# Optimization experiments

Hardware: AMD Instinct MI355X
Metric: run time of the kernel (lower is better)

The kernel has to match this reference:

```python
import jax, jax.numpy as jnp
import numpy as np

# Static problem constants (must match setup_inputs)
NUM_GRAPHS = 64      # batch_size = int(batch[-1]) + 1
PTS_PER_GRAPH = 512
RATIO = 16           # centroids per graph
HEADS = 4
IN_CH = 64           # = out_channels per head (concat=False -> mean over heads)
NEG_SLOPE = 0.2


def setup_inputs() -> dict:
    key = jax.random.key(0)
    ks = jax.random.split(key, 8)
    N = NUM_GRAPHS * PTS_PER_GRAPH
    x = jax.random.normal(ks[0], (N, IN_CH), dtype=jnp.float32)
    edge_index = jnp.zeros((2, 2), dtype=jnp.int64)  # unused by forward
    batch = (jnp.arange(N) // PTS_PER_GRAPH).astype(jnp.int64)
    xcent_base = jax.random.normal(ks[1], (RATIO, IN_CH), dtype=jnp.float32)
    W_l = jax.random.normal(ks[2], (IN_CH, HEADS * IN_CH), dtype=jnp.float32) / np.sqrt(IN_CH)
    b_l = jax.random.normal(ks[3], (HEADS * IN_CH,), dtype=jnp.float32) * 0.01
    W_r = jax.random.normal(ks[4], (IN_CH, HEADS * IN_CH), dtype=jnp.float32) / np.sqrt(IN_CH)
    b_r = jax.random.normal(ks[5], (HEADS * IN_CH,), dtype=jnp.float32) * 0.01
    att = jax.random.normal(ks[6], (HEADS, IN_CH), dtype=jnp.float32) / np.sqrt(IN_CH)
    bias = jax.random.normal(ks[7], (IN_CH,), dtype=jnp.float32) * 0.01
    return {"x": x, "edge_index": edge_index, "batch": batch,
            "xcent_base": xcent_base, "W_l": W_l, "b_l": b_l,
            "W_r": W_r, "b_r": b_r, "att": att, "bias": bias}


def _bipart_pool(x, batch, xcent_base, W_l, b_l, W_r, b_r, att, bias):
    N = x.shape[0]
    B = NUM_GRAPHS
    Nc = B * RATIO  # number of centroid (target) nodes

    # Dense bipartite edges: each source node -> all RATIO centroids of its graph.
    src = jnp.repeat(jnp.arange(N, dtype=jnp.int32), RATIO)                     # [E]
    dst = jnp.tile(jnp.arange(RATIO, dtype=jnp.int32), N) \
        + jnp.repeat(batch.astype(jnp.int32), RATIO) * RATIO                    # [E]

    # PyG GATv2Conv(add_self_loops=True): remove src==dst edges, then add
    # self loops (i,i) for i < min(N_src, N_dst) = Nc. Keep static shapes by
    # masking the removed edges instead of deleting them.
    self_idx = jnp.arange(Nc, dtype=jnp.int32)
    src_f = jnp.concatenate([src, self_idx])
    dst_f = jnp.concatenate([dst, self_idx])
    drop = jnp.concatenate([src == dst, jnp.zeros((Nc,), dtype=bool)])          # [E+Nc]

    # Linear projections (source and target sides)
    x_l = (x @ W_l + b_l).reshape(N, HEADS, IN_CH)                              # [N,H,C]
    xcent = jnp.tile(xcent_base, (B, 1))                                        # [Nc,IN]
    x_r = (xcent @ W_r + b_r).reshape(Nc, HEADS, IN_CH)                         # [Nc,H,C]

    # GATv2 attention: leaky_relu(x_i + x_j) . att, softmax per target node
    xj = x_l[src_f]                                                             # [E',H,C]
    g = jax.nn.leaky_relu(xj + x_r[dst_f], NEG_SLOPE)
    alpha = jnp.einsum('ehc,hc->eh', g, att)                                    # [E',H]
    alpha = jnp.where(drop[:, None], jnp.float32(-1e30), alpha)
    amax = jax.ops.segment_max(alpha, dst_f, num_segments=Nc)                   # [Nc,H]
    e = jnp.exp(alpha - amax[dst_f])
    den = jax.ops.segment_sum(e, dst_f, num_segments=Nc)                        # [Nc,H]
    w = e / den[dst_f]                                                          # [E',H]

    out = jax.ops.segment_sum(w[..., None] * xj, dst_f, num_segments=Nc)        # [Nc,H,C]
    out = out.mean(axis=1) + bias                                               # concat=False -> mean heads
    return out.reshape(B, RATIO, IN_CH)


def reference(x, edge_index, batch, xcent_base, W_l, b_l, W_r, b_r, att, bias):
    xcent = _bipart_pool(x, batch, xcent_base, W_l, b_l, W_r, b_r, att, bias)
    batchcent = jnp.repeat(jnp.arange(NUM_GRAPHS, dtype=jnp.int64), RATIO)
    return xcent, batchcent
```

## Files before the change

kernel.cpp:

```cpp
#include <hip/hip_runtime.h>

#define PTS 512
#define CH  64
#define NC  1024

using s8v = __attribute__((ext_vector_type(8))) short;
using f4v = __attribute__((ext_vector_type(4))) float;

static __device__ __forceinline__ unsigned short f2b(float f) {
    unsigned u = __float_as_uint(f);
    return (unsigned short)((u + 0x7FFFu + ((u >> 16) & 1u)) >> 16);
}
static __device__ __forceinline__ float b2f(unsigned short s) {
    return __uint_as_float((unsigned)s << 16);
}

__global__ __launch_bounds__(256) void k0(
    const float* __restrict__ xcb, const float* __restrict__ W_r,
    const float* __restrict__ b_r, const float* __restrict__ att,
    const float* __restrict__ W_l,
    float* __restrict__ xr_ws, float* __restrict__ sxr_ws,
    unsigned short* __restrict__ Wt)
{
    __shared__ float s_row[256];
    const int blk = blockIdx.x, tid = threadIdx.x;
    if (blk < 16) {
        const int h = blk >> 2, rq = blk & 3;
        const int rl = tid >> 6, c = tid & 63;
        const int r = rq * 4 + rl;
        float acc = b_r[h * 64 + c];
        for (int k = 0; k < 64; ++k)
            acc = fmaf(xcb[r * 64 + k], W_r[k * 256 + h * 64 + c], acc);
        xr_ws[(h * 16 + r) * 64 + c] = acc;
        s_row[rl * 64 + c] = acc;
        __syncthreads();
        if (tid < 4) {
            float s = 0.f;
            for (int cc = 0; cc < 64; ++cc)
                s = fmaf(s_row[tid * 64 + cc], att[h * 64 + cc], s);
            sxr_ws[h * 16 + rq * 4 + tid] = s;
        }
    } else {
        int base = (blk - 16) * 2048;
        for (int t = tid; t < 2048; t += 256) {
            int idx = base + t;
            int h = idx >> 12, ch = (idx >> 6) & 63, k = idx & 63;
            Wt[idx] = f2b(W_l[k * 256 + h * 64 + ch]);
        }
    }
}

__global__ __launch_bounds__(256, 2) void k1(
    const float* __restrict__ x, const unsigned short* __restrict__ Wt,
    const float* __restrict__ b_l, const float* __restrict__ att,
    const float* __restrict__ xr_ws, const float* __restrict__ sxr_ws,
    const float* __restrict__ bias,
    float* __restrict__ aws, unsigned short* __restrict__ xlself,
    float* __restrict__ out)
{
    __shared__ unsigned short s_xl[64 * 264];

    const int tid = threadIdx.x;
    const int lane = tid & 63;
    const int w = __builtin_amdgcn_readfirstlane(tid >> 6);
    const int blk = blockIdx.x;
    const int row0 = blk * 64;
    const int l15 = lane & 15, quad = lane >> 4;

    f4v acc[4][4];
    const f4v zf = {0.f, 0.f, 0.f, 0.f};
#pragma unroll
    for (int m = 0; m < 4; ++m)
#pragma unroll
        for (int n = 0; n < 4; ++n) acc[m][n] = zf;

#pragma unroll
    for (int ks = 0; ks < 2; ++ks) {
        s8v Af[4], Bf[4];
#pragma unroll
        for (int m = 0; m < 4; ++m) {
            const float* xp = x + (size_t)(row0 + m * 16 + l15) * 64 + ks * 32 + quad * 8;
            float4 u0 = *(const float4*)xp;
            float4 u1 = *(const float4*)(xp + 4);
            s8v a;
            a[0] = (short)f2b(u0.x); a[1] = (short)f2b(u0.y);
            a[2] = (short)f2b(u0.z); a[3] = (short)f2b(u0.w);
            a[4] = (short)f2b(u1.x); a[5] = (short)f2b(u1.y);
            a[6] = (short)f2b(u1.z); a[7] = (short)f2b(u1.w);
            Af[m] = a;
        }
#pragma unroll
        for (int n = 0; n < 4; ++n)
            Bf[n] = *(const s8v*)(Wt + (size_t)(w * 64 + n * 16 + l15) * 64
                                  + ks * 32 + quad * 8);
#pragma unroll
        for (int m = 0; m < 4; ++m)
#pragma unroll
            for (int n = 0; n < 4; ++n)
                acc[m][n] = __builtin_amdgcn_mfma_f32_16x16x32_bf16(
                    Af[m], Bf[n], acc[m][n], 0, 0, 0);
    }

    float blv[4];
#pragma unroll
    for (int n = 0; n < 4; ++n) blv[n] = b_l[w * 64 + n * 16 + l15];
#pragma unroll
    for (int m = 0; m < 4; ++m)
#pragma unroll
        for (int n = 0; n < 4; ++n) {
            int ch = w * 64 + n * 16 + l15;
#pragma unroll
            for (int qq = 0; qq < 4; ++qq) {
                int row = m * 16 + quad * 4 + qq;
                s_xl[row * 264 + ch] = f2b(acc[m][n][qq] + blv[n]);
            }
        }

    if (blk >= 16 && blk < 20) {
        int base = (blk - 16) * 16384;
        float bv = bias[tid & 63];
#pragma unroll
        for (int j = 0; j < 64; ++j) out[base + j * 256 + tid] = bv;
    }
    if (blk == 20) {
#pragma unroll
        for (int j = 0; j < 4; ++j) {
            int c = j * 256 + tid;
            out[65536 + c] = (float)(c >> 4);
        }
    }

    __syncthreads();

    if (blk < 16) {
#pragma unroll
        for (int t = 0; t < 8; ++t) {
            int idx = tid + t * 256;
            int row = idx >> 5, co = (idx & 31) * 8;
            uint4 v = *(const uint4*)&s_xl[row * 264 + co];
            *(uint4*)&xlself[(size_t)(row0 + row) * 256 + co] = v;
        }
    }

    const float* attw = att + w * 64;
    const float* xrw  = xr_ws + w * 1024;
    float ac[16];
#pragma unroll
    for (int r = 0; r < 16; ++r) ac[r] = 0.f;
    float sxl = 0.f;

#pragma unroll
    for (int half = 0; half < 2; ++half) {
        const int cb = half * 32;
        float xlv[32], atv[32];
#pragma unroll
        for (int c8 = 0; c8 < 4; ++c8) {
            uint4 raw = *(const uint4*)&s_xl[lane * 264 + w * 64 + cb + c8 * 8];
            unsigned uu[4] = {raw.x, raw.y, raw.z, raw.w};
#pragma unroll
            for (int p = 0; p < 4; ++p) {
                xlv[c8 * 8 + 2 * p]     = __uint_as_float(uu[p] << 16);
                xlv[c8 * 8 + 2 * p + 1] = __uint_as_float(uu[p] & 0xffff0000u);
            }
        }
#pragma unroll
        for (int cq = 0; cq < 8; ++cq) {
            float4 a4 = *(const float4*)(attw + cb + cq * 4);
            atv[cq * 4 + 0] = a4.x; atv[cq * 4 + 1] = a4.y;
            atv[cq * 4 + 2] = a4.z; atv[cq * 4 + 3] = a4.w;
        }
#pragma unroll
        for (int t = 0; t < 32; ++t) sxl = fmaf(atv[t], xlv[t], sxl);

#pragma unroll 2
        for (int r = 0; r < 16; ++r) {
            const float4* xrp = (const float4*)(xrw + r * 64 + cb);
            float a = 0.f;
#pragma unroll
            for (int cq = 0; cq < 8; ++cq) {
                float4 x4 = xrp[cq];
                a = fmaf(atv[cq * 4 + 0], fabsf(xlv[cq * 4 + 0] + x4.x), a);
                a = fmaf(atv[cq * 4 + 1], fabsf(xlv[cq * 4 + 1] + x4.y), a);
                a = fmaf(atv[cq * 4 + 2], fabsf(xlv[cq * 4 + 2] + x4.z), a);
                a = fmaf(atv[cq * 4 + 3], fabsf(xlv[cq * 4 + 3] + x4.w), a);
            }
            ac[r] += a;
        }
    }

    float* ap = aws + ((size_t)(blk >> 3) * 4 + w) * 8192 + (blk & 7) * 64 + lane;
#pragma unroll
    for (int r = 0; r < 16; ++r)
        ap[r * 512] = 0.6f * (sxl + sxr_ws[w * 16 + r]) + 0.4f * ac[r];
}

__global__ __launch_bounds__(512, 1) void k2(
    const float* __restrict__ x, const float* __restrict__ W_l,
    const float* __restrict__ b_l, const float* __restrict__ aws,
    const unsigned short* __restrict__ xlself, float* __restrict__ out)
{
    __shared__ float s_et[8192];
    __shared__ float sW[4096];
    __shared__ float s_y[1024];
    __shared__ float s_m[16], s_inv[16], s_f[16];

    const int bh = blockIdx.x, b = bh >> 2, h = bh & 3;
    const int tid = threadIdx.x;
    const float* abh = aws + (size_t)bh * 8192;

    for (int idx = tid; idx < 4096; idx += 512)
        sW[idx] = W_l[(idx >> 6) * 256 + h * 64 + (idx & 63)];
    for (int idx = tid; idx < 8192; idx += 512) {
        int r = idx >> 9, i = idx & 511;
        s_et[i * 16 + r] = abh[idx];
    }

    {
        const int r = tid >> 5, lg = tid & 31;
        const int snode = b * 16 + r;
        const float a_self = aws[(size_t)((snode >> 9) * 4 + h) * 8192
                                 + r * 512 + (snode & 511)];
        float m = a_self;
        for (int j = 0; j < 16; ++j) {
            int i = lg + j * 32;
            float a = abh[r * 512 + i];
            if (b == 0 && i == r) a = -1e30f;
            m = fmaxf(m, a);
        }
#pragma unroll
        for (int off = 16; off >= 1; off >>= 1) m = fmaxf(m, __shfl_xor(m, off));
        float d = 0.f;
        for (int j = 0; j < 16; ++j) {
            int i = lg + j * 32;
            float a = abh[r * 512 + i];
            d += (b == 0 && i == r) ? 0.f : __expf(a - m);
        }
#pragma unroll
        for (int off = 16; off >= 1; off >>= 1) d += __shfl_xor(d, off);
        if (lg == 0) {
            float es = __expf(a_self - m);
            float inv = 1.f / (d + es);
            s_m[r] = m; s_inv[r] = inv; s_f[r] = es * inv;
        }
    }
    __syncthreads();

    for (int idx = tid; idx < 8192; idx += 512) {
        int i = idx >> 4, r = idx & 15;
        float a = s_et[idx];
        float e = (b == 0 && i == r) ? 0.f : __expf(a - s_m[r]) * s_inv[r];
        s_et[idx] = e;
    }
    __syncthreads();

    const int kt = tid & 15, rt = (tid >> 4) & 3, is = tid >> 6;
    float y4[4][4];
#pragma unroll
    for (int i = 0; i < 4; ++i)
#pragma unroll
        for (int j = 0; j < 4; ++j) y4[i][j] = 0.f;

    const float* xb = x + ((size_t)b * PTS + is * 64) * 64;
#pragma unroll 4
    for (int ii = 0; ii < 64; ++ii) {
        float4 xv = *(const float4*)(xb + ii * 64 + kt * 4);
        float4 ev = *(const float4*)&s_et[(is * 64 + ii) * 16 + rt * 4];
        y4[0][0] = fmaf(ev.x, xv.x, y4[0][0]); y4[0][1] = fmaf(ev.x, xv.y, y4[0][1]);
        y4[0][2] = fmaf(ev.x, xv.z, y4[0][2]); y4[0][3] = fmaf(ev.x, xv.w, y4[0][3]);
        y4[1][0] = fmaf(ev.y, xv.x, y4[1][0]); y4[1][1] = fmaf(ev.y, xv.y, y4[1][1]);
        y4[1][2] = fmaf(ev.y, xv.z, y4[1][2]); y4[1][3] = fmaf(ev.y, xv.w, y4[1][3]);
        y4[2][0] = fmaf(ev.z, xv.x, y4[2][0]); y4[2][1] = fmaf(ev.z, xv.y, y4[2][1]);
        y4[2][2] = fmaf(ev.z, xv.z, y4[2][2]); y4[2][3] = fmaf(ev.z, xv.w, y4[2][3]);
        y4[3][0] = fmaf(ev.w, xv.x, y4[3][0]); y4[3][1] = fmaf(ev.w, xv.y, y4[3][1]);
        y4[3][2] = fmaf(ev.w, xv.z, y4[3][2]); y4[3][3] = fmaf(ev.w, xv.w, y4[3][3]);
    }
    __syncthreads();

#pragma unroll
    for (int rr = 0; rr < 4; ++rr)
        *(float4*)&s_et[is * 1024 + (rt * 4 + rr) * 64 + kt * 4] =
            make_float4(y4[rr][0], y4[rr][1], y4[rr][2], y4[rr][3]);
    __syncthreads();

    for (int o = tid; o < 1024; o += 512) {
        float s = 0.f;
#pragma unroll
        for (int sl = 0; sl < 8; ++sl) s += s_et[sl * 1024 + o];
        s_y[o] = s;
    }
    __syncthreads();

    for (int o = tid; o < 1024; o += 512) {
        int r = o >> 6, ch = o & 63;
        float a = 0.f;
#pragma unroll
        for (int k = 0; k < 64; ++k)
            a = fmaf(s_y[r * 64 + k], sW[k * 64 + ch], a);
        float f = s_f[r];
        float val = a + (1.f - f) * b_l[h * 64 + ch]
                  + f * b2f(xlself[(size_t)(b * 16 + r) * 256 + h * 64 + ch]);
        atomicAdd(&out[(b * 16 + r) * 64 + ch], 0.25f * val);
    }
}

extern "C" void kernel_launch(void* const* d_in, const int* in_sizes, int n_in,
                              void* d_out, int out_size, void* d_ws, size_t ws_size,
                              hipStream_t stream) {
    (void)in_sizes; (void)n_in; (void)out_size; (void)ws_size;
    const float* x    = (const float*)d_in[0];
    const float* xcb  = (const float*)d_in[3];
    const float* W_l  = (const float*)d_in[4];
    const float* b_l  = (const float*)d_in[5];
    const float* W_r  = (const float*)d_in[6];
    const float* b_r  = (const float*)d_in[7];
    const float* att  = (const float*)d_in[8];
    const float* bias = (const float*)d_in[9];
    float* out = (float*)d_out;

    float* wsf = (float*)d_ws;
    float*          aws    = wsf;
    float*          xr_ws  = wsf + 2097152;
    float*          sxr_ws = wsf + 2101248;
    unsigned short* Wt     = (unsigned short*)(wsf + 2101376);
    unsigned short* xlself = (unsigned short*)(wsf + 2109568);

    hipLaunchKernelGGL(k0, dim3(24), dim3(256), 0, stream,
                       xcb, W_r, b_r, att, W_l, xr_ws, sxr_ws, Wt);
    hipLaunchKernelGGL(k1, dim3(512), dim3(256), 0, stream,
                       x, Wt, b_l, att, xr_ws, sxr_ws, bias, aws, xlself, out);
    hipLaunchKernelGGL(k2, dim3(256), dim3(512), 0, stream,
                       x, W_l, b_l, aws, xlself, out);
}
```

Baseline: 119.3 us.

## Split k2 over four point-quarters per graph-head, reducing partials with atomics

k2 now launches 1024 blocks of 256 threads instead of 256 blocks of 512. Each block handles one quarter of the 512 source points for a (graph, head) pair, so more CUs are occupied and LDS use per block is smaller. Softmax statistics are computed redundantly in every quarter block, and the exponentials are written straight into LDS only for that quarter. The partial products are projected through W_l separately and combined via atomicAdd into the output, which adds 4x projection work and 4x atomics. The bias and self-loop terms are added only by quarter 0.

After: 133.8 us. +12.2%, slower.

```diff
diff --git a/kernel.cpp b/kernel.cpp
--- a/kernel.cpp
+++ b/kernel.cpp
@@ -194,62 +194,56 @@
         ap[r * 512] = 0.6f * (sxl + sxr_ws[w * 16 + r]) + 0.4f * ac[r];
 }
 
-__global__ __launch_bounds__(512, 1) void k2(
+__global__ __launch_bounds__(256, 4) void k2(
     const float* __restrict__ x, const float* __restrict__ W_l,
     const float* __restrict__ b_l, const float* __restrict__ aws,
     const unsigned short* __restrict__ xlself, float* __restrict__ out)
 {
-    __shared__ float s_et[8192];
+    __shared__ float s_et[2048];
+    __shared__ float s_p[3072];
     __shared__ float sW[4096];
-    __shared__ float s_y[1024];
-    __shared__ float s_m[16], s_inv[16], s_f[16];
-
-    const int bh = blockIdx.x, b = bh >> 2, h = bh & 3;
+    __shared__ float s_f[16];
+
+    const int q = blockIdx.x & 3, h = (blockIdx.x >> 2) & 3, b = blockIdx.x >> 4;
     const int tid = threadIdx.x;
-    const float* abh = aws + (size_t)bh * 8192;
-
-    for (int idx = tid; idx < 4096; idx += 512)
+    const float* abh = aws + (size_t)(b * 4 + h) * 8192;
+
+    for (int idx = tid; idx < 4096; idx += 256)
         sW[idx] = W_l[(idx >> 6) * 256 + h * 64 + (idx & 63)];
-    for (int idx = tid; idx < 8192; idx += 512) {
-        int r = idx >> 9, i = idx & 511;
-        s_et[i * 16 + r] = abh[idx];
-    }
 
     {
-        const int r = tid >> 5, lg = tid & 31;
+        const int r = tid >> 4, lg = tid & 15;
         const int snode = b * 16 + r;
         const float a_self = aws[(size_t)((snode >> 9) * 4 + h) * 8192
                                  + r * 512 + (snode & 511)];
         float m = a_self;
-        for (int j = 0; j < 16; ++j) {
-            int i = lg + j * 32;
+        for (int j = 0; j < 32; ++j) {
+            int i = lg + j * 16;
             float a = abh[r * 512 + i];
             if (b == 0 && i == r) a = -1e30f;
             m = fmaxf(m, a);
         }
 #pragma unroll
-        for (int off = 16; off >= 1; off >>= 1) m = fmaxf(m, __shfl_xor(m, off));
+        for (int off = 8; off >= 1; off >>= 1) m = fmaxf(m, __shfl_xor(m, off));
         float d = 0.f;
-        for (int j = 0; j < 16; ++j) {
-            int i = lg + j * 32;
+        for (int j = 0; j < 32; ++j) {
+            int i = lg + j * 16;
             float a = abh[r * 512 + i];
             d += (b == 0 && i == r) ? 0.f : __expf(a - m);
         }
 #pragma unroll
-        for (int off = 16; off >= 1; off >>= 1) d += __shfl_xor(d, off);
-        if (lg == 0) {
-            float es = __expf(a_self - m);
-            float inv = 1.f / (d + es);
-            s_m[r] = m; s_inv[r] = inv; s_f[r] = es * inv;
-        }
-    }
-    __syncthreads();
-
-    for (int idx = tid; idx < 8192; idx += 512) {
-        int i = idx >> 4, r = idx & 15;
-        float a = s_et[idx];
-        float e = (b == 0 && i == r) ? 0.f : __expf(a - s_m[r]) * s_inv[r];
-        s_et[idx] = e;
+        for (int off = 8; off >= 1; off >>= 1) d += __shfl_xor(d, off);
+        const float es = __expf(a_self - m);
+        const float inv = 1.f / (d + es);
+        if (lg == 0) s_f[r] = es * inv;
+
+        for (int j = 0; j < 8; ++j) {
+            int iloc = lg + j * 16;
+            int i = q * 128 + iloc;
+            float a = abh[r * 512 + i];
+            bool drop = (b == 0) && (i == r);
+            s_et[iloc * 16 + r] = drop ? 0.f : __expf(a - m) * inv;
+        }
     }
     __syncthreads();
 
@@ -260,11 +254,11 @@
 #pragma unroll
         for (int j = 0; j < 4; ++j) y4[i][j] = 0.f;
 
-    const float* xb = x + ((size_t)b * PTS + is * 64) * 64;
+    const float* xbq = x + ((size_t)b * PTS + q * 128 + is * 32) * 64;
 #pragma unroll 4
-    for (int ii = 0; ii < 64; ++ii) {
-        float4 xv = *(const float4*)(xb + ii * 64 + kt * 4);
-        float4 ev = *(const float4*)&s_et[(is * 64 + ii) * 16 + rt * 4];
+    for (int i = 0; i < 32; ++i) {
+        float4 xv = *(const float4*)(xbq + i * 64 + kt * 4);
+        float4 ev = *(const float4*)&s_et[(is * 32 + i) * 16 + rt * 4];
         y4[0][0] = fmaf(ev.x, xv.x, y4[0][0]); y4[0][1] = fmaf(ev.x, xv.y, y4[0][1]);
         y4[0][2] = fmaf(ev.x, xv.z, y4[0][2]); y4[0][3] = fmaf(ev.x, xv.w, y4[0][3]);
         y4[1][0] = fmaf(ev.y, xv.x, y4[1][0]); y4[1][1] = fmaf(ev.y, xv.y, y4[1][1]);
@@ -274,32 +268,53 @@
         y4[3][0] = fmaf(ev.w, xv.x, y4[3][0]); y4[3][1] = fmaf(ev.w, xv.y, y4[3][1]);
         y4[3][2] = fmaf(ev.w, xv.z, y4[3][2]); y4[3][3] = fmaf(ev.w, xv.w, y4[3][3]);
     }
+
+    if (is > 0) {
+#pragma unroll
+        for (int rr = 0; rr < 4; ++rr)
+            *(float4*)&s_p[((is - 1) * 64 + rt * 16 + kt) * 16 + rr * 4] =
+                make_float4(y4[rr][0], y4[rr][1], y4[rr][2], y4[rr][3]);
+    }
     __syncthreads();
-
-#pragma unroll
-    for (int rr = 0; rr < 4; ++rr)
-        *(float4*)&s_et[is * 1024 + (rt * 4 + rr) * 64 + kt * 4] =
-            make_float4(y4[rr][0], y4[rr][1], y4[rr][2], y4[rr][3]);
+    float* s_yq = s_et;
+    if (is == 0) {
+#pragma unroll
+        for (int j = 0; j < 3; ++j)
+#pragma unroll
+            for (int rr = 0; rr < 4; ++rr) {
+                float4 v = *(const float4*)&s_p[(j * 64 + rt * 16 + kt) * 16 + rr * 4];
+                y4[rr][0] += v.x; y4[rr][1] += v.y; y4[rr][2] += v.z; y4[rr][3] += v.w;
+            }
+#pragma unroll
+        for (int rr = 0; rr < 4; ++rr)
+            *(float4*)&s_yq[(rt * 4 + rr) * 64 + kt * 4] =
+                make_float4(y4[rr][0], y4[rr][1], y4[rr][2], y4[rr][3]);
+    }
     __syncthreads();
 
-    for (int o = tid; o < 1024; o += 512) {
-        float s = 0.f;
-#pragma unroll
-        for (int sl = 0; sl < 8; ++sl) s += s_et[sl * 1024 + o];
-        s_y[o] = s;
-    }
-    __syncthreads();
-
-    for (int o = tid; o < 1024; o += 512) {
-        int r = o >> 6, ch = o & 63;
-        float a = 0.f;
-#pragma unroll
-        for (int k = 0; k < 64; ++k)
-            a = fmaf(s_y[r * 64 + k], sW[k * 64 + ch], a);
-        float f = s_f[r];
-        float val = a + (1.f - f) * b_l[h * 64 + ch]
-                  + f * b2f(xlself[(size_t)(b * 16 + r) * 256 + h * 64 + ch]);
-        atomicAdd(&out[(b * 16 + r) * 64 + ch], 0.25f * val);
+    {
+        const int r2 = tid >> 4, ch = (tid & 15) * 4;
+        float o0 = 0.f, o1 = 0.f, o2 = 0.f, o3 = 0.f;
+#pragma unroll
+        for (int k = 0; k < 64; ++k) {
+            float yv = s_yq[r2 * 64 + k];
+            float4 wv = *(const float4*)&sW[k * 64 + ch];
+            o0 = fmaf(yv, wv.x, o0); o1 = fmaf(yv, wv.y, o1);
+            o2 = fmaf(yv, wv.z, o2); o3 = fmaf(yv, wv.w, o3);
+        }
+        if (q == 0) {
+            const float f = s_f[r2];
+            const float* blp = b_l + h * 64 + ch;
+            const unsigned short* xsp =
+                xlself + (size_t)(b * 16 + r2) * 256 + h * 64 + ch;
+            o0 += (1.f - f) * blp[0] + f * b2f(xsp[0]);
+            o1 += (1.f - f) * blp[1] + f * b2f(xsp[1]);
+            o2 += (1.f - f) * blp[2] + f * b2f(xsp[2]);
+            o3 += (1.f - f) * blp[3] + f * b2f(xsp[3]);
+        }
+        float* op = out + (b * 16 + r2) * 64 + ch;
+        atomicAdd(op + 0, 0.25f * o0); atomicAdd(op + 1, 0.25f * o1);
+        atomicAdd(op + 2, 0.25f * o2); atomicAdd(op + 3, 0.25f * o3);
     }
 }
 
@@ -328,6 +343,6 @@
                        xcb, W_r, b_r, att, W_l, xr_ws, sxr_ws, Wt);
     hipLaunchKernelGGL(k1, dim3(512), dim3(256), 0, stream,
                        x, Wt, b_l, att, xr_ws, sxr_ws, bias, aws, xlself, out);
-    hipLaunchKernelGGL(k2, dim3(256), dim3(512), 0, stream,
+    hipLaunchKernelGGL(k2, dim3(1024), dim3(256), 0, stream,
                        x, W_l, b_l, aws, xlself, out);
 }
```

## Fuse x_l projection and attention scoring into the per-(graph,head) softmax kernel

Applied to the files above, without the earlier changes.

Merges k1 and k2 into a single kernel launched per (graph, head). Each block recomputes its own x_l tile with MFMA and computes the attention logits locally. The self-loop x_l rows are computed in-block, so the xlself workspace round trip goes away, and the output bias initialisation moves into k0. This removes one launch and the cross-kernel dependency. In exchange, logits still pass through global memory within the block, the per-block work is serialised over two halves, and parallelism per block drops.

Measured after the change: 140.7 us. 1.18x slower.

```diff
diff --git a/kernel.cpp b/kernel.cpp
--- a/kernel.cpp
+++ b/kernel.cpp
@@ -11,16 +11,15 @@
     unsigned u = __float_as_uint(f);
     return (unsigned short)((u + 0x7FFFu + ((u >> 16) & 1u)) >> 16);
 }
-static __device__ __forceinline__ float b2f(unsigned short s) {
-    return __uint_as_float((unsigned)s << 16);
-}
+static __device__ __forceinline__ float blo(unsigned u) { return __uint_as_float(u << 16); }
+static __device__ __forceinline__ float bhi(unsigned u) { return __uint_as_float(u & 0xffff0000u); }
 
 __global__ __launch_bounds__(256) void k0(
     const float* __restrict__ xcb, const float* __restrict__ W_r,
     const float* __restrict__ b_r, const float* __restrict__ att,
-    const float* __restrict__ W_l,
+    const float* __restrict__ W_l, const float* __restrict__ bias,
     float* __restrict__ xr_ws, float* __restrict__ sxr_ws,
-    unsigned short* __restrict__ Wt)
+    unsigned short* __restrict__ Wt, float* __restrict__ out)
 {
     __shared__ float s_row[256];
     const int blk = blockIdx.x, tid = threadIdx.x;
@@ -40,46 +39,65 @@
                 s = fmaf(s_row[tid * 64 + cc], att[h * 64 + cc], s);
             sxr_ws[h * 16 + rq * 4 + tid] = s;
         }
-    } else {
+    } else if (blk < 24) {
         int base = (blk - 16) * 2048;
         for (int t = tid; t < 2048; t += 256) {
             int idx = base + t;
             int h = idx >> 12, ch = (idx >> 6) & 63, k = idx & 63;
             Wt[idx] = f2b(W_l[k * 256 + h * 64 + ch]);
         }
+    } else {
+        int base = (blk - 24) * 16384;
+        float bv = bias[tid & 63];
+#pragma unroll
+        for (int j = 0; j < 64; ++j) out[base + j * 256 + tid] = bv;
+        if (blk == 27) {
+#pragma unroll
+            for (int j = 0; j < 4; ++j) {
+                int c = j * 256 + tid;
+                out[65536 + c] = (float)(c >> 4);
+            }
+        }
     }
 }
 
-__global__ __launch_bounds__(256, 2) void k1(
+__global__ __launch_bounds__(512, 2) void kmain(
     const float* __restrict__ x, const unsigned short* __restrict__ Wt,
-    const float* __restrict__ b_l, const float* __restrict__ att,
+    const float* __restrict__ W_l, const float* __restrict__ b_l,
+    const float* __restrict__ att,
     const float* __restrict__ xr_ws, const float* __restrict__ sxr_ws,
-    const float* __restrict__ bias,
-    float* __restrict__ aws, unsigned short* __restrict__ xlself,
-    float* __restrict__ out)
+    float* __restrict__ aws, float* __restrict__ out)
 {
-    __shared__ unsigned short s_xl[64 * 264];
-
+    __shared__ float s_region[10240];
+    __shared__ float sW[4096];
+    __shared__ float s_xls[1024];
+    __shared__ float s_as[16], s_m[16], s_inv[16], s_f[16];
+
+    unsigned short* s_xl = (unsigned short*)s_region;
+    float* s_et = s_region;
+
+    const int bh = blockIdx.x, b = bh >> 2, h = bh & 3;
     const int tid = threadIdx.x;
     const int lane = tid & 63;
-    const int w = __builtin_amdgcn_readfirstlane(tid >> 6);
-    const int blk = blockIdx.x;
-    const int row0 = blk * 64;
+    const int w = tid >> 6;
     const int l15 = lane & 15, quad = lane >> 4;
-
-    f4v acc[4][4];
-    const f4v zf = {0.f, 0.f, 0.f, 0.f};
-#pragma unroll
-    for (int m = 0; m < 4; ++m)
-#pragma unroll
-        for (int n = 0; n < 4; ++n) acc[m][n] = zf;
-
-#pragma unroll
-    for (int ks = 0; ks < 2; ++ks) {
-        s8v Af[4], Bf[4];
-#pragma unroll
-        for (int m = 0; m < 4; ++m) {
-            const float* xp = x + (size_t)(row0 + m * 16 + l15) * 64 + ks * 32 + quad * 8;
+    float* awsb = aws + (size_t)bh * 8192;
+
+    for (int idx = tid; idx < 4096; idx += 512)
+        sW[idx] = W_l[(idx >> 6) * 256 + h * 64 + (idx & 63)];
+
+    float blv[4];
+#pragma unroll
+    for (int n = 0; n < 4; ++n) blv[n] = b_l[h * 64 + n * 16 + l15];
+
+    if (w == 0) {
+        f4v accs[4];
+        const f4v zf = {0.f, 0.f, 0.f, 0.f};
+#pragma unroll
+        for (int n = 0; n < 4; ++n) accs[n] = zf;
+#pragma unroll
+        for (int ks = 0; ks < 2; ++ks) {
+            const float* xp = x + (size_t)(b * 16 + l15) * 64 + ks * 32 + quad * 8;
             float4 u0 = *(const float4*)xp;
             float4 u1 = *(const float4*)(xp + 4);
             s8v a;
@@ -87,143 +105,154 @@
             a[2] = (short)f2b(u0.z); a[3] = (short)f2b(u0.w);
             a[4] = (short)f2b(u1.x); a[5] = (short)f2b(u1.y);
             a[6] = (short)f2b(u1.z); a[7] = (short)f2b(u1.w);
-            Af[m] = a;
+#pragma unroll
+            for (int n = 0; n < 4; ++n) {
+                s8v bv = *(const s8v*)(Wt + (size_t)(h * 64 + n * 16 + l15) * 64
+                                       + ks * 32 + quad * 8);
+                accs[n] = __builtin_amdgcn_mfma_f32_16x16x32_bf16(a, bv, accs[n], 0, 0, 0);
+            }
         }
 #pragma unroll
         for (int n = 0; n < 4; ++n)
-            Bf[n] = *(const s8v*)(Wt + (size_t)(w * 64 + n * 16 + l15) * 64
-                                  + ks * 32 + quad * 8);
-#pragma unroll
-        for (int m = 0; m < 4; ++m)
-#pragma unroll
-            for (int n = 0; n < 4; ++n)
-                acc[m][n] = __builtin_amdgcn_mfma_f32_16x16x32_bf16(
-                    Af[m], Bf[n], acc[m][n], 0, 0, 0);
-    }
-
-    float blv[4];
-#pragma unroll
-    for (int n = 0; n < 4; ++n) blv[n] = b_l[w * 64 + n * 16 + l15];
-#pragma unroll
-    for (int m = 0; m < 4; ++m)
-#pragma unroll
-        for (int n = 0; n < 4; ++n) {
-            int ch = w * 64 + n * 16 + l15;
-#pragma unroll
-            for (int qq = 0; qq < 4; ++qq) {
-                int row = m * 16 + quad * 4 + qq;
-                s_xl[row * 264 + ch] = f2b(acc[m][n][qq] + blv[n]);
-            }
-        }
-
-    if (blk >= 16 && blk < 20) {
-        int base = (blk - 16) * 16384;
-        float bv = bias[tid & 63];
-#pragma unroll
-        for (int j = 0; j < 64; ++j) out[base + j * 256 + tid] = bv;
-    }
-    if (blk == 20) {
-#pragma unroll
-        for (int j = 0; j < 4; ++j) {
-            int c = j * 256 + tid;
-            out[65536 + c] = (float)(c >> 4);
-        }
-    }
-
-    __syncthreads();
-
-    if (blk < 16) {
-#pragma unroll
-        for (int t = 0; t < 8; ++t) {
-            int idx = tid + t * 256;
-            int row = idx >> 5, co = (idx & 31) * 8;
-            uint4 v = *(const uint4*)&s_xl[row * 264 + co];
-            *(uint4*)&xlself[(size_t)(row0 + row) * 256 + co] = v;
-        }
-    }
-
-    const float* attw = att + w * 64;
-    const float* xrw  = xr_ws + w * 1024;
-    float ac[16];
-#pragma unroll
-    for (int r = 0; r < 16; ++r) ac[r] = 0.f;
-    float sxl = 0.f;
-
-#pragma unroll
-    for (int half = 0; half < 2; ++half) {
-        const int cb = half * 32;
-        float xlv[32], atv[32];
-#pragma unroll
-        for (int c8 = 0; c8 < 4; ++c8) {
-            uint4 raw = *(const uint4*)&s_xl[lane * 264 + w * 64 + cb + c8 * 8];
-            unsigned uu[4] = {raw.x, raw.y, raw.z, raw.w};
-#pragma unroll
-            for (int p = 0; p < 4; ++p) {
-                xlv[c8 * 8 + 2 * p]     = __uint_as_float(uu[p] << 16);
-                xlv[c8 * 8 + 2 * p + 1] = __uint_as_float(uu[p] & 0xffff0000u);
-            }
-        }
-#pragma unroll
-        for (int cq = 0; cq < 8; ++cq) {
-            float4 a4 = *(const float4*)(attw + cb + cq * 4);
-            atv[cq * 4 + 0] = a4.x; atv[cq * 4 + 1] = a4.y;
-            atv[cq * 4 + 2] = a4.z; atv[cq * 4 + 3] = a4.w;
-        }
-#pragma unroll
-        for (int t = 0; t < 32; ++t) sxl = fmaf(atv[t], xlv[t], sxl);
-
+#pragma unroll
+            for (int qq = 0; qq < 4; ++qq)
+                s_xls[(quad * 4 + qq) * 64 + n * 16 + l15] = accs[n][qq] + blv[n];
+    }
+
+    const float* attw = att + h * 64;
+    const float* xrw  = xr_ws + h * 1024;
+
+#pragma unroll 1
+    for (int hg = 0; hg < 2; ++hg) {
+        {
+            f4v acc[2][4];
+            const f4v zf = {0.f, 0.f, 0.f, 0.f};
+#pragma unroll
+            for (int m = 0; m < 2; ++m)
+#pragma unroll
+                for (int n = 0; n < 4; ++n) acc[m][n] = zf;
+#pragma unroll
+            for (int ks = 0; ks < 2; ++ks) {
+                s8v Af[2], Bf[4];
+#pragma unroll
+                for (int m = 0; m < 2; ++m) {
+                    const float* xp = x + (size_t)(b * 512 + hg * 256 + w * 32
+                                     + m * 16 + l15) * 64 + ks * 32 + quad * 8;
+                    float4 u0 = *(const float4*)xp;
+                    float4 u1 = *(const float4*)(xp + 4);
+                    s8v a;
+                    a[0] = (short)f2b(u0.x); a[1] = (short)f2b(u0.y);
+                    a[2] = (short)f2b(u0.z); a[3] = (short)f2b(u0.w);
+                    a[4] = (short)f2b(u1.x); a[5] = (short)f2b(u1.y);
+                    a[6] = (short)f2b(u1.z); a[7] = (short)f2b(u1.w);
+                    Af[m] = a;
+                }
+#pragma unroll
+                for (int n = 0; n < 4; ++n)
+                    Bf[n] = *(const s8v*)(Wt + (size_t)(h * 64 + n * 16 + l15) * 64
+                                          + ks * 32 + quad * 8);
+#pragma unroll
+                for (int m = 0; m < 2; ++m)
+#pragma unroll
+                    for (int n = 0; n < 4; ++n)
+                        acc[m][n] = __builtin_amdgcn_mfma_f32_16x16x32_bf16(
+                            Af[m], Bf[n], acc[m][n], 0, 0, 0);
+            }
+#pragma unroll
+            for (int m = 0; m < 2; ++m)
+#pragma unroll
+                for (int n = 0; n < 4; ++n) {
+                    int ch = n * 16 + l15;
+#pragma unroll
+                    for (int qq = 0; qq < 4; ++qq) {
+                        int row = w * 32 + m * 16 + quad * 4 + qq;
+                        s_xl[row * 72 + ch] = f2b(acc[m][n][qq] + blv[n]);
+                    }
+                }
+        }
+        __syncthreads();
+
+        {
+            const int i_loc = tid >> 1, halfc = tid & 1, cb = halfc * 32;
+            float xlv[32], atv[32];
+#pragma unroll
+            for (int c8 = 0; c8 < 4; ++c8) {
+                uint4 raw = *(const uint4*)&s_xl[i_loc * 72 + cb + c8 * 8];
+                unsigned uu[4] = {raw.x, raw.y, raw.z, raw.w};
+#pragma unroll
+                for (int p = 0; p < 4; ++p) {
+                    xlv[c8 * 8 + 2 * p]     = blo(uu[p]);
+                    xlv[c8 * 8 + 2 * p + 1] = bhi(uu[p]);
+                }
+            }
+#pragma unroll
+            for (int cq = 0; cq < 8; ++cq) {
+                float4 a4 = *(const float4*)(attw + cb + cq * 4);
+                atv[cq * 4 + 0] = a4.x; atv[cq * 4 + 1] = a4.y;
+                atv[cq * 4 + 2] = a4.z; atv[cq * 4 + 3] = a4.w;
+            }
+            float sxl = 0.f;
+#pragma unroll
+            for (int t = 0; t < 32; ++t) sxl = fmaf(atv[t], xlv[t], sxl);
+
+            float ac[16];
+#pragma unroll
+            for (int r = 0; r < 16; ++r) ac[r] = 0.f;
 #pragma unroll 2
-        for (int r = 0; r < 16; ++r) {
-            const float4* xrp = (const float4*)(xrw + r * 64 + cb);
-            float a = 0.f;
-#pragma unroll
-            for (int cq = 0; cq < 8; ++cq) {
-                float4 x4 = xrp[cq];
-                a = fmaf(atv[cq * 4 + 0], fabsf(xlv[cq * 4 + 0] + x4.x), a);
-                a = fmaf(atv[cq * 4 + 1], fabsf(xlv[cq * 4 + 1] + x4.y), a);
-                a = fmaf(atv[cq * 4 + 2], fabsf(xlv[cq * 4 + 2] + x4.z), a);
-                a = fmaf(atv[cq * 4 + 3], fabsf(xlv[cq * 4 + 3] + x4.w), a);
-            }
-            ac[r] += a;
-        }
-    }
-
-    float* ap = aws + ((size_t)(blk >> 3) * 4 + w) * 8192 + (blk & 7) * 64 + lane;
-#pragma unroll
-    for (int r = 0; r < 16; ++r)
-        ap[r * 512] = 0.6f * (sxl + sxr_ws[w * 16 + r]) + 0.4f * ac[r];
-}
-
-__global__ __launch_bounds__(512, 1) void k2(
-    const float* __restrict__ x, const float* __restrict__ W_l,
-    const float* __restrict__ b_l, const float* __restrict__ aws,
-    const unsigned short* __restrict__ xlself, float* __restrict__ out)
-{
-    __shared__ float s_et[8192];
-    __shared__ float sW[4096];
-    __shared__ float s_y[1024];
-    __shared__ float s_m[16], s_inv[16], s_f[16];
-
-    const int bh = blockIdx.x, b = bh >> 2, h = bh & 3;
-    const int tid = threadIdx.x;
-    const float* abh = aws + (size_t)bh * 8192;
-
-    for (int idx = tid; idx < 4096; idx += 512)
-        sW[idx] = W_l[(idx >> 6) * 256 + h * 64 + (idx & 63)];
-    for (int idx = tid; idx < 8192; idx += 512) {
-        int r = idx >> 9, i = idx & 511;
-        s_et[i * 16 + r] = abh[idx];
-    }
+            for (int r = 0; r < 16; ++r) {
+                const float4* xrp = (const float4*)(xrw + r * 64 + cb);
+                float a = 0.f;
+#pragma unroll
+                for (int cq = 0; cq < 8; ++cq) {
+                    float4 x4 = xrp[cq];
+                    a = fmaf(atv[cq * 4 + 0], fabsf(xlv[cq * 4 + 0] + x4.x), a);
+                    a = fmaf(atv[cq * 4 + 1], fabsf(xlv[cq * 4 + 1] + x4.y), a);
+                    a = fmaf(atv[cq * 4 + 2], fabsf(xlv[cq * 4 + 2] + x4.z), a);
+                    a = fmaf(atv[cq * 4 + 3], fabsf(xlv[cq * 4 + 3] + x4.w), a);
+                }
+                ac[r] = a;
+            }
+            sxl += __shfl_xor(sxl, 1);
+#pragma unroll
+            for (int r = 0; r < 16; ++r) ac[r] += __shfl_xor(ac[r], 1);
+
+            const int i = hg * 256 + i_loc;
+            float* ap = awsb + (halfc * 8) * 512 + i;
+#pragma unroll
+            for (int r8 = 0; r8 < 8; ++r8) {
+                int r = halfc * 8 + r8;
+                ap[r8 * 512] = 0.6f * (sxl + sxr_ws[h * 16 + r]) + 0.4f * ac[r];
+            }
+        }
+        __syncthreads();
+    }
+
+    if (tid < 16) {
+        int r = tid;
+        float sxl_s = 0.f, acs = 0.f;
+#pragma unroll
+        for (int cq = 0; cq < 16; ++cq) {
+            float4 v4 = *(const float4*)&s_xls[r * 64 + cq * 4];
+            float4 a4 = *(const float4*)(attw + cq * 4);
+            float4 x4 = *(const float4*)(xrw + r * 64 + cq * 4);
+            sxl_s = fmaf(a4.x, v4.x, sxl_s); sxl_s = fmaf(a4.y, v4.y, sxl_s);
+            sxl_s = fmaf(a4.z, v4.z, sxl_s); sxl_s = fmaf(a4.w, v4.w, sxl_s);
+            acs = fmaf(a4.x, fabsf(v4.x + x4.x), acs);
+            acs = fmaf(a4.y, fabsf(v4.y + x4.y), acs);
+            acs = fmaf(a4.z, fabsf(v4.z + x4.z), acs);
+            acs = fmaf(a4.w, fabsf(v4.w + x4.w), acs);
+        }
+        s_as[r] = 0.6f * (sxl_s + sxr_ws[h * 16 + r]) + 0.4f * acs;
+    }
+    __syncthreads();
 
     {
         const int r = tid >> 5, lg = tid & 31;
-        const int snode = b * 16 + r;
-        const float a_self = aws[(size_t)((snode >> 9) * 4 + h) * 8192
-                                 + r * 512 + (snode & 511)];
+        const float a_self = s_as[r];
         float m = a_self;
         for (int j = 0; j < 16; ++j) {
             int i = lg + j * 32;
-            float a = abh[r * 512 + i];
+            float a = awsb[r * 512 + i];
             if (b == 0 && i == r) a = -1e30f;
             m = fmaxf(m, a);
         }
@@ -232,7 +261,7 @@
         float d = 0.f;
         for (int j = 0; j < 16; ++j) {
             int i = lg + j * 32;
-            float a = abh[r * 512 + i];
+            float a = awsb[r * 512 + i];
             d += (b == 0 && i == r) ? 0.f : __expf(a - m);
         }
 #pragma unroll
@@ -243,13 +272,20 @@
             s_m[r] = m; s_inv[r] = inv; s_f[r] = es * inv;
         }
     }
+    {
+        const int r = tid & 15, i0 = tid >> 4;
+        for (int k = 0; k < 16; ++k) {
+            int i = i0 + k * 32;
+            s_et[i * 20 + r] = awsb[r * 512 + i];
+        }
+    }
     __syncthreads();
 
     for (int idx = tid; idx < 8192; idx += 512) {
         int i = idx >> 4, r = idx & 15;
-        float a = s_et[idx];
+        float a = s_et[i * 20 + r];
         float e = (b == 0 && i == r) ? 0.f : __expf(a - s_m[r]) * s_inv[r];
-        s_et[idx] = e;
+        s_et[i * 20 + r] = e;
     }
     __syncthreads();
 
@@ -264,7 +300,7 @@
 #pragma unroll 4
     for (int ii = 0; ii < 64; ++ii) {
         float4 xv = *(const float4*)(xb + ii * 64 + kt * 4);
-        float4 ev = *(const float4*)&s_et[(is * 64 + ii) * 16 + rt * 4];
+        float4 ev = *(const float4*)&s_et[(is * 64 + ii) * 20 + rt * 4];
         y4[0][0] = fmaf(ev.x, xv.x, y4[0][0]); y4[0][1] = fmaf(ev.x, xv.y, y4[0][1]);
         y4[0][2] = fmaf(ev.x, xv.z, y4[0][2]); y4[0][3] = fmaf(ev.x, xv.w, y4[0][3]);
         y4[1][0] = fmaf(ev.y, xv.x, y4[1][0]); y4[1][1] = fmaf(ev.y, xv.y, y4[1][1]);
@@ -278,15 +314,15 @@
 
 #pragma unroll
     for (int rr = 0; rr < 4; ++rr)
-        *(float4*)&s_et[is * 1024 + (rt * 4 + rr) * 64 + kt * 4] =
+        *(float4*)&s_region[is * 1024 + (rt * 4 + rr) * 64 + kt * 4] =
             make_float4(y4[rr][0], y4[rr][1], y4[rr][2], y4[rr][3]);
     __syncthreads();
 
     for (int o = tid; o < 1024; o += 512) {
         float s = 0.f;
 #pragma unroll
-        for (int sl = 0; sl < 8; ++sl) s += s_et[sl * 1024 + o];
-        s_y[o] = s;
+        for (int sl = 0; sl < 8; ++sl) s += s_region[sl * 1024 + o];
+        s_region[8192 + o] = s;
     }
     __syncthreads();
 
@@ -295,10 +331,9 @@
         float a = 0.f;
 #pragma unroll
         for (int k = 0; k < 64; ++k)
-            a = fmaf(s_y[r * 64 + k], sW[k * 64 + ch], a);
+            a = fmaf(s_region[8192 + r * 64 + k], sW[k * 64 + ch], a);
         float f = s_f[r];
-        float val = a + (1.f - f) * b_l[h * 64 + ch]
-                  + f * b2f(xlself[(size_t)(b * 16 + r) * 256 + h * 64 + ch]);
+        float val = a + (1.f - f) * b_l[h * 64 + ch] + f * s_xls[r * 64 + ch];
         atomicAdd(&out[(b * 16 + r) * 64 + ch], 0.25f * val);
     }
 }
@@ -322,12 +357,9 @@
     float*          xr_ws  = wsf + 2097152;
     float*          sxr_ws = wsf + 2101248;
     unsigned short* Wt     = (unsigned short*)(wsf + 2101376);
-    unsigned short* xlself = (unsigned short*)(wsf + 2109568);
-
-    hipLaunchKernelGGL(k0, dim3(24), dim3(256), 0, stream,
-                       xcb, W_r, b_r, att, W_l, xr_ws, sxr_ws, Wt);
-    hipLaunchKernelGGL(k1, dim3(512), dim3(256), 0, stream,
-                       x, Wt, b_l, att, xr_ws, sxr_ws, bias, aws, xlself, out);
-    hipLaunchKernelGGL(k2, dim3(256), dim3(512), 0, stream,
-                       x, W_l, b_l, aws, xlself, out);
+
+    hipLaunchKernelGGL(k0, dim3(28), dim3(256), 0, stream,
+                       xcb, W_r, b_r, att, W_l, bias, xr_ws, sxr_ws, Wt, out);
+    hipLaunchKernelGGL(kmain, dim3(256), dim3(512), 0, stream,
+                       x, Wt, W_l, b_l, att, xr_ws, sxr_ws, aws, out);
 }
```

## Compute partial softmax max/sum in k1 and merge online in k2

Applied to the files above, without the earlier changes.

k1 now computes per-chunk max and exp-sum for each target row with wavefront reductions and writes them to new workspace buffers. k2 merges these partials with an online-softmax combine instead of reading the attention logits twice to find the max and denominator. The transpose into shared memory now uses a padded stride of 20 to cut LDS bank conflicts. In exchange k1 does extra shuffles and exps in its epilogue, and k2 uses more shared memory.

New measurement: 125.8 us. 1.06x slower.

```diff
diff --git a/kernel.cpp b/kernel.cpp
--- a/kernel.cpp
+++ b/kernel.cpp
@@ -56,7 +56,8 @@
     const float* __restrict__ xr_ws, const float* __restrict__ sxr_ws,
     const float* __restrict__ bias,
     float* __restrict__ aws, unsigned short* __restrict__ xlself,
-    float* __restrict__ out)
+    float* __restrict__ out,
+    float* __restrict__ sm_ws, float* __restrict__ ss_ws)
 {
     __shared__ unsigned short s_xl[64 * 264];
 
@@ -188,18 +189,40 @@
         }
     }
 
-    float* ap = aws + ((size_t)(blk >> 3) * 4 + w) * 8192 + (blk & 7) * 64 + lane;
-#pragma unroll
-    for (int r = 0; r < 16; ++r)
-        ap[r * 512] = 0.6f * (sxl + sxr_ws[w * 16 + r]) + 0.4f * ac[r];
+    float av[16];
+    const int bh = (blk >> 3) * 4 + w, chunk = blk & 7;
+    float* ap = aws + (size_t)bh * 8192 + chunk * 64 + lane;
+#pragma unroll
+    for (int r = 0; r < 16; ++r) {
+        av[r] = 0.6f * (sxl + sxr_ws[w * 16 + r]) + 0.4f * ac[r];
+        ap[r * 512] = av[r];
+    }
+
+    const bool maskblk = (row0 == 0);
+#pragma unroll 2
+    for (int r = 0; r < 16; ++r) {
+        float v = (maskblk && lane == r) ? -1e30f : av[r];
+        float m = v;
+#pragma unroll
+        for (int off = 32; off >= 1; off >>= 1) m = fmaxf(m, __shfl_xor(m, off));
+        float e = __expf(v - m);
+        float s = e;
+#pragma unroll
+        for (int off = 32; off >= 1; off >>= 1) s += __shfl_xor(s, off);
+        if (lane == r) {
+            sm_ws[((size_t)bh * 16 + r) * 8 + chunk] = m;
+            ss_ws[((size_t)bh * 16 + r) * 8 + chunk] = s;
+        }
+    }
 }
 
 __global__ __launch_bounds__(512, 1) void k2(
     const float* __restrict__ x, const float* __restrict__ W_l,
     const float* __restrict__ b_l, const float* __restrict__ aws,
+    const float* __restrict__ sm_ws, const float* __restrict__ ss_ws,
     const unsigned short* __restrict__ xlself, float* __restrict__ out)
 {
-    __shared__ float s_et[8192];
+    __shared__ float s_et[10240];
     __shared__ float sW[4096];
     __shared__ float s_y[1024];
     __shared__ float s_m[16], s_inv[16], s_f[16];
@@ -208,48 +231,39 @@
     const int tid = threadIdx.x;
     const float* abh = aws + (size_t)bh * 8192;
 
+    if (tid < 128) {
+        const int r = tid >> 3, c = tid & 7;
+        float m = sm_ws[((size_t)bh * 16 + r) * 8 + c];
+        float s = ss_ws[((size_t)bh * 16 + r) * 8 + c];
+#pragma unroll
+        for (int off = 1; off < 8; off <<= 1) {
+            float m2 = __shfl_xor(m, off);
+            float s2 = __shfl_xor(s, off);
+            float mm = fmaxf(m, m2);
+            s = s * __expf(m - mm) + s2 * __expf(m2 - mm);
+            m = mm;
+        }
+        if (c == 0) {
+            const int snode = b * 16 + r;
+            const float a_self = aws[(size_t)((snode >> 9) * 4 + h) * 8192
+                                     + r * 512 + (snode & 511)];
+            float mm = fmaxf(m, a_self);
+            float es = __expf(a_self - mm);
+            float den = s * __expf(m - mm) + es;
+            float inv = 1.f / den;
+            s_m[r] = mm; s_inv[r] = inv; s_f[r] = es * inv;
+        }
+    }
     for (int idx = tid; idx < 4096; idx += 512)
         sW[idx] = W_l[(idx >> 6) * 256 + h * 64 + (idx & 63)];
-    for (int idx = tid; idx < 8192; idx += 512) {
-        int r = idx >> 9, i = idx & 511;
-        s_et[i * 16 + r] = abh[idx];
-    }
-
-    {
-        const int r = tid >> 5, lg = tid & 31;
-        const int snode = b * 16 + r;
-        const float a_self = aws[(size_t)((snode >> 9) * 4 + h) * 8192
-                                 + r * 512 + (snode & 511)];
-        float m = a_self;
-        for (int j = 0; j < 16; ++j) {
-            int i = lg + j * 32;
-            float a = abh[r * 512 + i];
-            if (b == 0 && i == r) a = -1e30f;
-            m = fmaxf(m, a);
-        }
-#pragma unroll
-        for (int off = 16; off >= 1; off >>= 1) m = fmaxf(m, __shfl_xor(m, off));
-        float d = 0.f;
-        for (int j = 0; j < 16; ++j) {
-            int i = lg + j * 32;
-            float a = abh[r * 512 + i];
-            d += (b == 0 && i == r) ? 0.f : __expf(a - m);
-        }
-#pragma unroll
-        for (int off = 16; off >= 1; off >>= 1) d += __shfl_xor(d, off);
-        if (lg == 0) {
-            float es = __expf(a_self - m);
-            float inv = 1.f / (d + es);
-            s_m[r] = m; s_inv[r] = inv; s_f[r] = es * inv;
-        }
-    }
-    __syncthreads();
-
-    for (int idx = tid; idx < 8192; idx += 512) {
-        int i = idx >> 4, r = idx & 15;
-        float a = s_et[idx];
+    __syncthreads();
+
+    for (int k = 0; k < 16; ++k) {
+        int idx = k * 512 + tid;
+        int r = k, i = tid;
+        float a = abh[idx];
         float e = (b == 0 && i == r) ? 0.f : __expf(a - s_m[r]) * s_inv[r];
-        s_et[idx] = e;
+        s_et[i * 20 + r] = e;
     }
     __syncthreads();
 
@@ -264,7 +278,7 @@
 #pragma unroll 4
     for (int ii = 0; ii < 64; ++ii) {
         float4 xv = *(const float4*)(xb + ii * 64 + kt * 4);
-        float4 ev = *(const float4*)&s_et[(is * 64 + ii) * 16 + rt * 4];
+        float4 ev = *(const float4*)&s_et[(is * 64 + ii) * 20 + rt * 4];
         y4[0][0] = fmaf(ev.x, xv.x, y4[0][0]); y4[0][1] = fmaf(ev.x, xv.y, y4[0][1]);
         y4[0][2] = fmaf(ev.x, xv.z, y4[0][2]); y4[0][3] = fmaf(ev.x, xv.w, y4[0][3]);
         y4[1][0] = fmaf(ev.y, xv.x, y4[1][0]); y4[1][1] = fmaf(ev.y, xv.y, y4[1][1]);
@@ -323,11 +337,14 @@
     float*          sxr_ws = wsf + 2101248;
     unsigned short* Wt     = (unsigned short*)(wsf + 2101376);
     unsigned short* xlself = (unsigned short*)(wsf + 2109568);
+    float*          sm_ws  = wsf + 2240640;
+    float*          ss_ws  = wsf + 2273408;
 
     hipLaunchKernelGGL(k0, dim3(24), dim3(256), 0, stream,
                        xcb, W_r, b_r, att, W_l, xr_ws, sxr_ws, Wt);
     hipLaunchKernelGGL(k1, dim3(512), dim3(256), 0, stream,
-                       x, Wt, b_l, att, xr_ws, sxr_ws, bias, aws, xlself, out);
+                       x, Wt, b_l, att, xr_ws, sxr_ws, bias, aws, xlself, out,
+                       sm_ws, ss_ws);
     hipLaunchKernelGGL(k2, dim3(256), dim3(512), 0, stream,
-                       x, W_l, b_l, aws, xlself, out);
-}
+                       x, W_l, b_l, aws, sm_ws, ss_ws, xlself, out);
+}
```
